# Optimization experiments

Measured on AMD Instinct MI355X. Metric: run time of the kernel, lower is better.

Reference implementation:

```python
import jax, jax.numpy as jnp
import numpy as np

EPS = 1e-8  # torch cosine_similarity default eps


def _l2_normalize(v):
    n = jnp.linalg.norm(v, axis=-1, keepdims=True)
    return v / jnp.maximum(n, EPS)


def setup_inputs() -> dict:
    key = jax.random.key(0)
    kx, km = jax.random.split(key)
    x = jax.random.normal(kx, (65536, 1024), dtype=jnp.float32)
    memory = jax.random.normal(km, (40, 1024), dtype=jnp.float32)
    return {"x": x, "memory": memory, "top_k": 5}


def reference(x, memory, top_k):
    # Cosine similarity [N, M] without materializing the N x M x D broadcast:
    # normalize rows, then a single GEMM.
    xn = _l2_normalize(x)            # [N, D]
    mn = _l2_normalize(memory)       # [M, D]
    sims = jnp.einsum('nd,md->nm', xn, mn)  # [N, M]
    # memory pool size (40) >= top_k, so the original takes top-k indices
    # (descending) and returns the prototype for the top-1 match.
    _, idx = jax.lax.top_k(sims, top_k)     # [N, top_k]
    nearest = memory[idx[:, 0]]             # [N, D]
    return (nearest, x)
```

## Files before the change

kernel.cpp:

```cpp
#include <hip/hip_runtime.h>


#define DIM 1024
#define NMEM 40

typedef float  vf4 __attribute__((ext_vector_type(4)));
typedef float  f4a __attribute__((ext_vector_type(4)));
typedef short  s8v __attribute__((ext_vector_type(8)));

union FragU { s8v v; unsigned int u[4]; };

constexpr float TAU = 2.5e-4f;

__global__ __launch_bounds__(64) void k_norms(const float* __restrict__ mem,
                                              double* __restrict__ inv64,
                                              float* __restrict__ inv32) {
  const int m = blockIdx.x;
  const int lane = threadIdx.x;
  const float* __restrict__ row = mem + (size_t)m * DIM;
  double s = 0.0;
#pragma unroll
  for (int i = 0; i < DIM / 64; ++i) {
    double v = (double)row[lane + 64 * i];
    s = fma(v, v, s);
  }
#pragma unroll
  for (int off = 32; off > 0; off >>= 1) s += __shfl_xor(s, off, 64);
  if (lane == 0) {
    double n = sqrt(s);
    n = (n > 1e-8) ? n : 1e-8;
    inv64[m] = 1.0 / n;
    inv32[m] = (float)(1.0 / n);
  }
}

__global__ __launch_bounds__(256) void k_prep(const float* __restrict__ mem,
                                              const float* __restrict__ inv32,
                                              unsigned short* __restrict__ BH,
                                              unsigned short* __restrict__ BL) {
  const int m = blockIdx.x;
  const int k0 = threadIdx.x * 4;
#pragma unroll
  for (int j = 0; j < 4; ++j) {
    const int k = k0 + j;
    const size_t dst = (size_t)(k >> 5) * (48 * 32) + (size_t)m * 32 + (k & 31);
    if (m < NMEM) {
      const float s = inv32[m];
      float w = mem[(size_t)m * DIM + k] * s;
      unsigned int u = __builtin_bit_cast(unsigned int, w);
      BH[dst] = (unsigned short)(u >> 16);
      float hf = __builtin_bit_cast(float, u & 0xFFFF0000u);
      float lo = w - hf;
      BL[dst] = (unsigned short)(__builtin_bit_cast(unsigned int, lo) >> 16);
    } else {
      BH[dst] = 0;
      BL[dst] = 0;
    }
  }
}

__global__ __launch_bounds__(256, 2) void k_main(const float* __restrict__ x,
                                                 const float* __restrict__ mem,
                                                 const unsigned short* __restrict__ BH,
                                                 const unsigned short* __restrict__ BL,
                                                 float* __restrict__ out_near,
                                                 float* __restrict__ out_x,
                                                 unsigned int* __restrict__ flagbits) {
  __shared__ vf4 xq4[4 * 16 * 64];

  const int tid  = threadIdx.x;
  const int lane = tid & 63;
  const int w    = __builtin_amdgcn_readfirstlane(tid >> 6);
  const int row  = lane & 15;
  const int kg   = lane >> 4;
  const int rowbase = blockIdx.x * 64 + w * 16;

  const unsigned short* __restrict__ bp = BH + row * 32 + kg * 8;
  const unsigned short* __restrict__ lp = BL + row * 32 + kg * 8;

  f4a acc[3];
#pragma unroll
  for (int t = 0; t < 3; ++t) acc[t] = (f4a){0.f, 0.f, 0.f, 0.f};
  float nx = 0.f;

  const int q0 = (blockIdx.x + w) & 3;
  vf4* __restrict__ xw = xq4 + w * 1024;

#pragma unroll 1
  for (int qq = 0; qq < 4; ++qq) {
    const int q = (q0 + qq) & 3;
    vf4 g[16];
#pragma unroll
    for (int r = 0; r < 16; ++r)
      g[r] = *(const vf4*)(x + (size_t)(rowbase + r) * DIM + q * 256 + lane * 4);
#pragma unroll
    for (int r = 0; r < 16; ++r) {
      __builtin_nontemporal_store(g[r],
          (vf4*)(out_x + (size_t)(rowbase + r) * DIM + q * 256 + lane * 4));
      xw[r * 64 + (lane ^ (r & 7))] = g[r];
    }
#pragma unroll
    for (int tl = 0; tl < 8; ++tl) {
      const int T = q * 8 + tl;
      s8v bh[3], bl[3];
#pragma unroll
      for (int tt = 0; tt < 3; ++tt) {
        bh[tt] = *(const s8v*)(bp + (size_t)T * 1536 + tt * 512);
        bl[tt] = *(const s8v*)(lp + (size_t)T * 1536 + tt * 512);
      }
      const int f = tl * 8 + kg * 2;
      vf4 a0 = xw[row * 64 + (f ^ (row & 7))];
      vf4 a1 = xw[row * 64 + ((f + 1) ^ (row & 7))];
      nx = fmaf(a0.x, a0.x, fmaf(a0.y, a0.y, fmaf(a0.z, a0.z, fmaf(a0.w, a0.w, nx))));
      nx = fmaf(a1.x, a1.x, fmaf(a1.y, a1.y, fmaf(a1.z, a1.z, fmaf(a1.w, a1.w, nx))));
      FragU ah, al;
      {
        float fbuf[8] = {a0.x, a0.y, a0.z, a0.w, a1.x, a1.y, a1.z, a1.w};
#pragma unroll
        for (int p = 0; p < 4; ++p) {
          unsigned int u0 = __builtin_bit_cast(unsigned int, fbuf[2 * p]);
          unsigned int u1 = __builtin_bit_cast(unsigned int, fbuf[2 * p + 1]);
          ah.u[p] = (u1 & 0xFFFF0000u) | (u0 >> 16);
          float h0 = __builtin_bit_cast(float, u0 & 0xFFFF0000u);
          float h1 = __builtin_bit_cast(float, u1 & 0xFFFF0000u);
          float l0 = fbuf[2 * p] - h0;
          float l1 = fbuf[2 * p + 1] - h1;
          al.u[p] = (__builtin_bit_cast(unsigned int, l1) & 0xFFFF0000u) |
                    (__builtin_bit_cast(unsigned int, l0) >> 16);
        }
      }
#pragma unroll
      for (int tt = 0; tt < 3; ++tt) {
        acc[tt] = __builtin_amdgcn_mfma_f32_16x16x32_bf16(ah.v, bh[tt], acc[tt], 0, 0, 0);
        acc[tt] = __builtin_amdgcn_mfma_f32_16x16x32_bf16(ah.v, bl[tt], acc[tt], 0, 0, 0);
        acc[tt] = __builtin_amdgcn_mfma_f32_16x16x32_bf16(al.v, bh[tt], acc[tt], 0, 0, 0);
        acc[tt] = __builtin_amdgcn_mfma_f32_16x16x32_bf16(al.v, bl[tt], acc[tt], 0, 0, 0);
      }
    }
  }

  nx += __shfl_xor(nx, 16, 64);
  nx += __shfl_xor(nx, 32, 64);

  float v1[4], v2[4];
  int   i1[4];
#pragma unroll
  for (int j = 0; j < 4; ++j) {
    float c0 = acc[0][j], c1 = acc[1][j];
    float c2 = (row < 8) ? acc[2][j] : -3.4e38f;
    float a1 = c0, a2 = -3.4e38f;
    int   ai = row;
    if (c1 > a1) { a2 = a1; a1 = c1; ai = row + 16; } else a2 = c1;
    if (c2 > a1) { a2 = a1; a1 = c2; ai = row + 32; } else if (c2 > a2) a2 = c2;
    v1[j] = a1; v2[j] = a2; i1[j] = ai;
  }
#pragma unroll
  for (int st = 1; st < 16; st <<= 1) {
#pragma unroll
    for (int j = 0; j < 4; ++j) {
      float o1 = __shfl_xor(v1[j], st, 64);
      float o2 = __shfl_xor(v2[j], st, 64);
      int   oi = __shfl_xor(i1[j], st, 64);
      if (o1 > v1[j]) { v2[j] = fmaxf(v1[j], o2); v1[j] = o1; i1[j] = oi; }
      else            { v2[j] = fmaxf(v2[j], o1); }
    }
  }
  const int g = lane >> 4;
  float nx0 = __shfl(nx, 4 * g + 0, 64);
  float nx1 = __shfl(nx, 4 * g + 1, 64);
  float nx2 = __shfl(nx, 4 * g + 2, 64);
  float nx3 = __shfl(nx, 4 * g + 3, 64);
  int fl0 = !((v1[0] - v2[0]) * rsqrtf(fmaxf(nx0, 1e-30f)) >= TAU);
  int fl1 = !((v1[1] - v2[1]) * rsqrtf(fmaxf(nx1, 1e-30f)) >= TAU);
  int fl2 = !((v1[2] - v2[2]) * rsqrtf(fmaxf(nx2, 1e-30f)) >= TAU);
  int fl3 = !((v1[3] - v2[3]) * rsqrtf(fmaxf(nx3, 1e-30f)) >= TAU);
  const int srcl = 16 * ((lane & 15) >> 2);
  int f0 = __shfl(fl0, srcl, 64);
  int f1 = __shfl(fl1, srcl, 64);
  int f2 = __shfl(fl2, srcl, 64);
  int f3 = __shfl(fl3, srcl, 64);
  const int jsel = lane & 3;
  int flv = (jsel & 2) ? ((jsel & 1) ? f3 : f2) : ((jsel & 1) ? f1 : f0);
  unsigned long long bmask = __ballot(flv != 0);
  if (lane == 0) flagbits[blockIdx.x * 4 + w] = (unsigned int)(bmask & 0xFFFFull);

  const vf4* __restrict__ m4 = (const vf4*)mem;
#pragma unroll
  for (int r = 0; r < 16; ++r) {
    int am = __shfl(i1[r & 3], 16 * (r >> 2), 64);
    am = __builtin_amdgcn_readfirstlane(am);
    const vf4* __restrict__ src = m4 + (size_t)am * (DIM / 4);
    vf4* __restrict__ dst = (vf4*)out_near + (size_t)(rowbase + r) * (DIM / 4);
#pragma unroll
    for (int j = 0; j < 4; ++j) {
      vf4 v = src[lane + 64 * j];
      __builtin_nontemporal_store(v, &dst[lane + 64 * j]);
    }
  }
}

__global__ __launch_bounds__(256) void k_refine(const float* __restrict__ x,
                                                const float* __restrict__ mem,
                                                const double* __restrict__ inv64,
                                                const unsigned int* __restrict__ flagbits,
                                                float* __restrict__ out_near) {
  unsigned int mask = flagbits[blockIdx.x];
  if (mask == 0u) return;
  const int tid = threadIdx.x;
  const int lane = tid & 63;
  const int wid = tid >> 6;
  __shared__ double bval[4];
  __shared__ int bidx[4];
  while (mask) {
    int r = __ffs(mask) - 1;
    mask &= (mask - 1u);
    int rrow = blockIdx.x * 16 + r;
    const float* __restrict__ xr = x + (size_t)rrow * DIM;
    double xd[16];
#pragma unroll
    for (int i = 0; i < 16; ++i) xd[i] = (double)xr[lane + 64 * i];
    double best = -1e300;
    int bi = 0;
    for (int q = 0; q < 10; ++q) {
      int m = wid * 10 + q;
      const float* __restrict__ mr = mem + (size_t)m * DIM;
      double s = 0.0;
#pragma unroll
      for (int i = 0; i < 16; ++i) s = fma(xd[i], (double)mr[lane + 64 * i], s);
#pragma unroll
      for (int off = 32; off > 0; off >>= 1) s += __shfl_xor(s, off, 64);
      double v = s * inv64[m];
      if (v > best) { best = v; bi = m; }
    }
    if (lane == 0) { bval[wid] = best; bidx[wid] = bi; }
    __syncthreads();
    double gv = bval[0];
    int gi = bidx[0];
#pragma unroll
    for (int gg = 1; gg < 4; ++gg) {
      if (bval[gg] > gv) { gv = bval[gg]; gi = bidx[gg]; }
    }
    const float4* __restrict__ src = (const float4*)mem + (size_t)gi * (DIM / 4);
    float4* __restrict__ dst = (float4*)out_near + (size_t)rrow * (DIM / 4);
    dst[tid] = src[tid];
    __syncthreads();
  }
}

extern "C" void kernel_launch(void* const* d_in, const int* in_sizes, int n_in,
                              void* d_out, int out_size, void* d_ws, size_t ws_size,
                              hipStream_t stream) {
  const float* x   = (const float*)d_in[0];
  const float* mem = (const float*)d_in[1];

  const int n_rows = in_sizes[0] / DIM;
  float* out_near = (float*)d_out;
  float* out_x    = (float*)d_out + (size_t)n_rows * DIM;

  double* inv64 = (double*)d_ws;
  float*  inv32 = (float*)((char*)d_ws + 320);
  unsigned int* flagbits = (unsigned int*)((char*)d_ws + 512);
  unsigned short* BH = (unsigned short*)((char*)d_ws + 32768);
  unsigned short* BL = (unsigned short*)((char*)d_ws + 131072);

  hipLaunchKernelGGL(k_norms, dim3(NMEM), dim3(64), 0, stream, mem, inv64, inv32);
  hipLaunchKernelGGL(k_prep,  dim3(48),   dim3(256), 0, stream, mem, inv32, BH, BL);
  hipLaunchKernelGGL(k_main,  dim3(n_rows / 64), dim3(256), 0, stream,
                     x, mem, BH, BL, out_near, out_x, flagbits);
  hipLaunchKernelGGL(k_refine, dim3(n_rows / 16), dim3(256), 0, stream,
                     x, mem, inv64, flagbits, out_near);
}
```

Measured before the change: 188.6 us.

## Halve per-stage x chunk to float2 and raise occupancy to four blocks per CU

Each wave now stages x in eight 128-column chunks of float2 instead of four 256-column chunks of float4. This halves the register staging array and the LDS tile, and the LDS layout switches from an XOR swizzle to a padded row stride of 66. Launch bounds go from 2 to 4 blocks per SM so more waves can hide global-memory latency. The costs are narrower global loads and stores, more loop iterations, and tighter register limits that could cause spilling.

```diff
diff --git a/kernel.cpp b/kernel.cpp
--- a/kernel.cpp
+++ b/kernel.cpp
@@ -5,6 +5,7 @@
 #define NMEM 40
 
 typedef float  vf4 __attribute__((ext_vector_type(4)));
+typedef float  vf2 __attribute__((ext_vector_type(2)));
 typedef float  f4a __attribute__((ext_vector_type(4)));
 typedef short  s8v __attribute__((ext_vector_type(8)));
 
@@ -59,14 +60,14 @@
   }
 }
 
-__global__ __launch_bounds__(256, 2) void k_main(const float* __restrict__ x,
+__global__ __launch_bounds__(256, 4) void k_main(const float* __restrict__ x,
                                                  const float* __restrict__ mem,
                                                  const unsigned short* __restrict__ BH,
                                                  const unsigned short* __restrict__ BL,
                                                  float* __restrict__ out_near,
                                                  float* __restrict__ out_x,
                                                  unsigned int* __restrict__ flagbits) {
-  __shared__ vf4 xq4[4 * 16 * 64];
+  __shared__ vf2 xw8[4 * 16 * 66];
 
   const int tid  = threadIdx.x;
   const int lane = tid & 63;
@@ -83,39 +84,41 @@
   for (int t = 0; t < 3; ++t) acc[t] = (f4a){0.f, 0.f, 0.f, 0.f};
   float nx = 0.f;
 
-  const int q0 = (blockIdx.x + w) & 3;
-  vf4* __restrict__ xw = xq4 + w * 1024;
+  const int e0 = (blockIdx.x + w * 3) & 7;
+  vf2* __restrict__ xw = xw8 + w * 1056;
 
 #pragma unroll 1
-  for (int qq = 0; qq < 4; ++qq) {
-    const int q = (q0 + qq) & 3;
-    vf4 g[16];
+  for (int ee = 0; ee < 8; ++ee) {
+    const int e = (e0 + ee) & 7;
+    vf2 g[16];
 #pragma unroll
     for (int r = 0; r < 16; ++r)
-      g[r] = *(const vf4*)(x + (size_t)(rowbase + r) * DIM + q * 256 + lane * 4);
+      g[r] = *(const vf2*)(x + (size_t)(rowbase + r) * DIM + e * 128 + lane * 2);
 #pragma unroll
     for (int r = 0; r < 16; ++r) {
       __builtin_nontemporal_store(g[r],
-          (vf4*)(out_x + (size_t)(rowbase + r) * DIM + q * 256 + lane * 4));
-      xw[r * 64 + (lane ^ (r & 7))] = g[r];
-    }
-#pragma unroll
-    for (int tl = 0; tl < 8; ++tl) {
-      const int T = q * 8 + tl;
+          (vf2*)(out_x + (size_t)(rowbase + r) * DIM + e * 128 + lane * 2));
+      xw[r * 66 + lane] = g[r];
+    }
+#pragma unroll
+    for (int tl = 0; tl < 4; ++tl) {
+      const int T = e * 4 + tl;
       s8v bh[3], bl[3];
 #pragma unroll
       for (int tt = 0; tt < 3; ++tt) {
         bh[tt] = *(const s8v*)(bp + (size_t)T * 1536 + tt * 512);
         bl[tt] = *(const s8v*)(lp + (size_t)T * 1536 + tt * 512);
       }
-      const int f = tl * 8 + kg * 2;
-      vf4 a0 = xw[row * 64 + (f ^ (row & 7))];
-      vf4 a1 = xw[row * 64 + ((f + 1) ^ (row & 7))];
-      nx = fmaf(a0.x, a0.x, fmaf(a0.y, a0.y, fmaf(a0.z, a0.z, fmaf(a0.w, a0.w, nx))));
-      nx = fmaf(a1.x, a1.x, fmaf(a1.y, a1.y, fmaf(a1.z, a1.z, fmaf(a1.w, a1.w, nx))));
+      const int fb = tl * 16 + kg * 4;
+      vf2 p0 = xw[row * 66 + fb + 0];
+      vf2 p1 = xw[row * 66 + fb + 1];
+      vf2 p2 = xw[row * 66 + fb + 2];
+      vf2 p3 = xw[row * 66 + fb + 3];
+      nx = fmaf(p0.x, p0.x, fmaf(p0.y, p0.y, fmaf(p1.x, p1.x, fmaf(p1.y, p1.y, nx))));
+      nx = fmaf(p2.x, p2.x, fmaf(p2.y, p2.y, fmaf(p3.x, p3.x, fmaf(p3.y, p3.y, nx))));
       FragU ah, al;
       {
-        float fbuf[8] = {a0.x, a0.y, a0.z, a0.w, a1.x, a1.y, a1.z, a1.w};
+        float fbuf[8] = {p0.x, p0.y, p1.x, p1.y, p2.x, p2.y, p3.x, p3.y};
 #pragma unroll
         for (int p = 0; p < 4; ++p) {
           unsigned int u0 = __builtin_bit_cast(unsigned int, fbuf[2 * p]);
```

After: 208.6 us. 1.11x slower.

## Software-pipeline x chunk loads and batch B-fragment loads across quarter iterations

Applied to the files above, without the earlier changes.

Moves the global load of the next 256-column chunk of x ahead of the MFMA work for the current chunk, so HBM reads overlap with compute instead of stalling at the top of each iteration. The B high/low fragments are loaded in two batches of four k-tiles rather than one tile at a time, and the MFMA order is regrouped so the low×low products come after the other three. This raises register pressure (16 prefetched vf4 plus 24 s8v fragments), which may cut occupancy or cause spills.

```diff
diff --git a/kernel.cpp b/kernel.cpp
--- a/kernel.cpp
+++ b/kernel.cpp
@@ -86,28 +86,36 @@
   const int q0 = (blockIdx.x + w) & 3;
   vf4* __restrict__ xw = xq4 + w * 1024;
 
+  vf4 g[16];
+#pragma unroll
+  for (int r = 0; r < 16; ++r)
+    g[r] = *(const vf4*)(x + (size_t)(rowbase + r) * DIM + q0 * 256 + lane * 4);
+
 #pragma unroll 1
   for (int qq = 0; qq < 4; ++qq) {
     const int q = (q0 + qq) & 3;
-    vf4 g[16];
-#pragma unroll
-    for (int r = 0; r < 16; ++r)
-      g[r] = *(const vf4*)(x + (size_t)(rowbase + r) * DIM + q * 256 + lane * 4);
+    s8v bh[4][3], bl[4][3];
+#pragma unroll
+    for (int tl = 0; tl < 4; ++tl)
+#pragma unroll
+      for (int tt = 0; tt < 3; ++tt) {
+        bh[tl][tt] = *(const s8v*)(bp + (size_t)(q * 8 + tl) * 1536 + tt * 512);
+        bl[tl][tt] = *(const s8v*)(lp + (size_t)(q * 8 + tl) * 1536 + tt * 512);
+      }
 #pragma unroll
     for (int r = 0; r < 16; ++r) {
       __builtin_nontemporal_store(g[r],
           (vf4*)(out_x + (size_t)(rowbase + r) * DIM + q * 256 + lane * 4));
       xw[r * 64 + (lane ^ (r & 7))] = g[r];
     }
-#pragma unroll
-    for (int tl = 0; tl < 8; ++tl) {
-      const int T = q * 8 + tl;
-      s8v bh[3], bl[3];
-#pragma unroll
-      for (int tt = 0; tt < 3; ++tt) {
-        bh[tt] = *(const s8v*)(bp + (size_t)T * 1536 + tt * 512);
-        bl[tt] = *(const s8v*)(lp + (size_t)T * 1536 + tt * 512);
-      }
+    if (qq < 3) {
+      const int qn = (q0 + qq + 1) & 3;
+#pragma unroll
+      for (int r = 0; r < 16; ++r)
+        g[r] = *(const vf4*)(x + (size_t)(rowbase + r) * DIM + qn * 256 + lane * 4);
+    }
+#pragma unroll
+    for (int tl = 0; tl < 4; ++tl) {
       const int f = tl * 8 + kg * 2;
       vf4 a0 = xw[row * 64 + (f ^ (row & 7))];
       vf4 a1 = xw[row * 64 + ((f + 1) ^ (row & 7))];
@@ -115,27 +123,69 @@
       nx = fmaf(a1.x, a1.x, fmaf(a1.y, a1.y, fmaf(a1.z, a1.z, fmaf(a1.w, a1.w, nx))));
       FragU ah, al;
       {
-        float fbuf[8] = {a0.x, a0.y, a0.z, a0.w, a1.x, a1.y, a1.z, a1.w};
+        float fb[8] = {a0.x, a0.y, a0.z, a0.w, a1.x, a1.y, a1.z, a1.w};
 #pragma unroll
         for (int p = 0; p < 4; ++p) {
-          unsigned int u0 = __builtin_bit_cast(unsigned int, fbuf[2 * p]);
-          unsigned int u1 = __builtin_bit_cast(unsigned int, fbuf[2 * p + 1]);
+          unsigned int u0 = __builtin_bit_cast(unsigned int, fb[2 * p]);
+          unsigned int u1 = __builtin_bit_cast(unsigned int, fb[2 * p + 1]);
           ah.u[p] = (u1 & 0xFFFF0000u) | (u0 >> 16);
           float h0 = __builtin_bit_cast(float, u0 & 0xFFFF0000u);
           float h1 = __builtin_bit_cast(float, u1 & 0xFFFF0000u);
-          float l0 = fbuf[2 * p] - h0;
-          float l1 = fbuf[2 * p + 1] - h1;
+          float l0 = fb[2 * p] - h0;
+          float l1 = fb[2 * p + 1] - h1;
           al.u[p] = (__builtin_bit_cast(unsigned int, l1) & 0xFFFF0000u) |
                     (__builtin_bit_cast(unsigned int, l0) >> 16);
         }
       }
 #pragma unroll
       for (int tt = 0; tt < 3; ++tt) {
-        acc[tt] = __builtin_amdgcn_mfma_f32_16x16x32_bf16(ah.v, bh[tt], acc[tt], 0, 0, 0);
-        acc[tt] = __builtin_amdgcn_mfma_f32_16x16x32_bf16(ah.v, bl[tt], acc[tt], 0, 0, 0);
-        acc[tt] = __builtin_amdgcn_mfma_f32_16x16x32_bf16(al.v, bh[tt], acc[tt], 0, 0, 0);
-        acc[tt] = __builtin_amdgcn_mfma_f32_16x16x32_bf16(al.v, bl[tt], acc[tt], 0, 0, 0);
-      }
+        acc[tt] = __builtin_amdgcn_mfma_f32_16x16x32_bf16(ah.v, bh[tl][tt], acc[tt], 0, 0, 0);
+        acc[tt] = __builtin_amdgcn_mfma_f32_16x16x32_bf16(ah.v, bl[tl][tt], acc[tt], 0, 0, 0);
+        acc[tt] = __builtin_amdgcn_mfma_f32_16x16x32_bf16(al.v, bh[tl][tt], acc[tt], 0, 0, 0);
+      }
+#pragma unroll
+      for (int tt = 0; tt < 3; ++tt)
+        acc[tt] = __builtin_amdgcn_mfma_f32_16x16x32_bf16(al.v, bl[tl][tt], acc[tt], 0, 0, 0);
+    }
+#pragma unroll
+    for (int tl = 0; tl < 4; ++tl)
+#pragma unroll
+      for (int tt = 0; tt < 3; ++tt) {
+        bh[tl][tt] = *(const s8v*)(bp + (size_t)(q * 8 + 4 + tl) * 1536 + tt * 512);
+        bl[tl][tt] = *(const s8v*)(lp + (size_t)(q * 8 + 4 + tl) * 1536 + tt * 512);
+      }
+#pragma unroll
+    for (int tl = 0; tl < 4; ++tl) {
+      const int f = (4 + tl) * 8 + kg * 2;
+      vf4 a0 = xw[row * 64 + (f ^ (row & 7))];
+      vf4 a1 = xw[row * 64 + ((f + 1) ^ (row & 7))];
+      nx = fmaf(a0.x, a0.x, fmaf(a0.y, a0.y, fmaf(a0.z, a0.z, fmaf(a0.w, a0.w, nx))));
+      nx = fmaf(a1.x, a1.x, fmaf(a1.y, a1.y, fmaf(a1.z, a1.z, fmaf(a1.w, a1.w, nx))));
+      FragU ah, al;
+      {
+        float fb[8] = {a0.x, a0.y, a0.z, a0.w, a1.x, a1.y, a1.z, a1.w};
+#pragma unroll
+        for (int p = 0; p < 4; ++p) {
+          unsigned int u0 = __builtin_bit_cast(unsigned int, fb[2 * p]);
+          unsigned int u1 = __builtin_bit_cast(unsigned int, fb[2 * p + 1]);
+          ah.u[p] = (u1 & 0xFFFF0000u) | (u0 >> 16);
+          float h0 = __builtin_bit_cast(float, u0 & 0xFFFF0000u);
+          float h1 = __builtin_bit_cast(float, u1 & 0xFFFF0000u);
+          float l0 = fb[2 * p] - h0;
+          float l1 = fb[2 * p + 1] - h1;
+          al.u[p] = (__builtin_bit_cast(unsigned int, l1) & 0xFFFF0000u) |
+                    (__builtin_bit_cast(unsigned int, l0) >> 16);
+        }
+      }
+#pragma unroll
+      for (int tt = 0; tt < 3; ++tt) {
+        acc[tt] = __builtin_amdgcn_mfma_f32_16x16x32_bf16(ah.v, bh[tl][tt], acc[tt], 0, 0, 0);
+        acc[tt] = __builtin_amdgcn_mfma_f32_16x16x32_bf16(ah.v, bl[tl][tt], acc[tt], 0, 0, 0);
+        acc[tt] = __builtin_amdgcn_mfma_f32_16x16x32_bf16(al.v, bh[tl][tt], acc[tt], 0, 0, 0);
+      }
+#pragma unroll
+      for (int tt = 0; tt < 3; ++tt)
+        acc[tt] = __builtin_amdgcn_mfma_f32_16x16x32_bf16(al.v, bl[tl][tt], acc[tt], 0, 0, 0);
     }
   }
 
@@ -165,11 +215,11 @@
       else            { v2[j] = fmaxf(v2[j], o1); }
     }
   }
-  const int g = lane >> 4;
-  float nx0 = __shfl(nx, 4 * g + 0, 64);
-  float nx1 = __shfl(nx, 4 * g + 1, 64);
-  float nx2 = __shfl(nx, 4 * g + 2, 64);
-  float nx3 = __shfl(nx, 4 * g + 3, 64);
+  const int gidx = lane >> 4;
+  float nx0 = __shfl(nx, 4 * gidx + 0, 64);
+  float nx1 = __shfl(nx, 4 * gidx + 1, 64);
+  float nx2 = __shfl(nx, 4 * gidx + 2, 64);
+  float nx3 = __shfl(nx, 4 * gidx + 3, 64);
   int fl0 = !((v1[0] - v2[0]) * rsqrtf(fmaxf(nx0, 1e-30f)) >= TAU);
   int fl1 = !((v1[1] - v2[1]) * rsqrtf(fmaxf(nx1, 1e-30f)) >= TAU);
   int fl2 = !((v1[2] - v2[2]) * rsqrtf(fmaxf(nx2, 1e-30f)) >= TAU);
```

Measured after the change: 183.6 us. 1.03x faster.
